# Performance work log

Hardware: AMD Instinct MI355X
Metric: run time of the kernel (lower is better)

## Reference

```python
import jax, jax.numpy as jnp
import numpy as np

B, S, D_IN, D_OUT, NUM_LAYERS = 128, 64, 2048, 2048, 64

def setup_inputs() -> dict:
    key = jax.random.key(0)
    k1, k2, k3 = jax.random.split(key, 3)
    x = jax.random.normal(k1, (B, S, D_IN), dtype=jnp.float32)
    weight = jax.random.normal(k2, (NUM_LAYERS, D_OUT, D_IN), dtype=jnp.float32)
    layer_idx = jax.random.randint(k3, (S,), 0, NUM_LAYERS, dtype=jnp.int32)
    return {"x": x, "weight": weight, "layer_idx": layer_idx}

def reference(x, weight, layer_idx):
    # x: [B, S, D_in]; weight: [L, D_out, D_in]; layer_idx: [S] ints in [0, L)
    # Per position s: out[:, s, :] = x[:, s, :] @ weight[layer_idx[s]].T
    w_sel = weight[layer_idx]                      # [S, D_out, D_in] gather
    out = jnp.einsum('bsd,sod->bso', x, w_sel)     # batched per-position GEMMs
    return out
```

## Files before the change

### kernel.cpp

```cpp
#include <hip/hip_runtime.h>
#include <hip/hip_bf16.h>

#define B_DIM 128
#define S_DIM 64
#define DIN   2048
#define DOUT  2048
#define NLAYERS 64

#define BM 128
#define BN 128
#define BK 64
#define NK (DIN / BK)
#define NTILES (S_DIM * (DOUT / BN))
#define NXCD 8

typedef __bf16 bf16_t;
typedef __attribute__((ext_vector_type(8))) bf16_t bf16x8;
typedef __attribute__((ext_vector_type(4))) float f32x4;

__global__ void rank_sort(const int* __restrict__ layer_idx, int* __restrict__ perm) {
    __shared__ int L[S_DIM];
    const int s = threadIdx.x;
    L[s] = layer_idx[s];
    __syncthreads();
    const int mine = L[s];
    int rank = 0;
    #pragma unroll
    for (int t = 0; t < S_DIM; ++t) {
        const int lt = L[t];
        rank += (lt < mine || (lt == mine && t < s)) ? 1 : 0;
    }
    perm[rank] = s;
}

__launch_bounds__(256, 2)
__global__ void flex_linear_gemm(const float* __restrict__ x,
                                 const float* __restrict__ w,
                                 const int* __restrict__ layer_idx,
                                 const int* __restrict__ perm,
                                 float* __restrict__ out) {
    __shared__ bf16_t Alds[BM * BK];
    __shared__ bf16_t Blds[BN * BK];

    const int orig = blockIdx.x;
    const int xcd  = orig & (NXCD - 1);
    const int slot = orig >> 3;
    const int tile = xcd * (NTILES / NXCD) + slot;
    const int yy   = tile >> 4;
    const int nb   = tile & 15;

    const int s  = perm[yy];
    const int layer = layer_idx[s];

    const float* Ag = x + (size_t)s * DIN;
    const float* Bg = w + (size_t)layer * (size_t)(DOUT * DIN) + (size_t)(nb * BN) * DIN;

    const int tid  = threadIdx.x;
    const int lane = tid & 63;
    const int wave = tid >> 6;
    const int wr = (wave >> 1) * 64;
    const int wc = (wave & 1) * 64;
    const int lrow = lane & 15;
    const int lk   = (lane >> 4) * 8;

    int offW[4];
    const float* pA[4];
    const float* pB[4];
    #pragma unroll
    for (int i = 0; i < 4; ++i) {
        const int row = (tid >> 3) + 32 * i;
        const int kc8 = (tid & 7) * 8;
        offW[i] = (row * BK + kc8) ^ ((row & 7) << 3);
        pA[i] = Ag + (size_t)row * (S_DIM * DIN) + kc8;
        pB[i] = Bg + (size_t)row * DIN + kc8;
    }
    int offA[2][4], offB[2][4];
    #pragma unroll
    for (int kk = 0; kk < 2; ++kk) {
        #pragma unroll
        for (int m = 0; m < 4; ++m) {
            const int ra = wr + m * 16 + lrow;
            const int rb = wc + m * 16 + lrow;
            offA[kk][m] = (ra * BK + kk * 32 + lk) ^ ((ra & 7) << 3);
            offB[kk][m] = (rb * BK + kk * 32 + lk) ^ ((rb & 7) << 3);
        }
    }

    f32x4 RA[8], RB[8];
    f32x4 acc[4][4] = {};

    auto issue = [&](int kb) {
        const int koff = kb * BK;
        #pragma unroll
        for (int i = 0; i < 4; ++i) {
            const float* a = pA[i] + koff;
            const float* b = pB[i] + koff;
            RA[2 * i]     = *(const f32x4*)a;
            RA[2 * i + 1] = *(const f32x4*)(a + 4);
            RB[2 * i]     = *(const f32x4*)b;
            RB[2 * i + 1] = *(const f32x4*)(b + 4);
        }
    };
    auto cvt_write = [&]() {
        #pragma unroll
        for (int i = 0; i < 4; ++i) {
            bf16x8 va, vb;
            #pragma unroll
            for (int j = 0; j < 4; ++j) {
                va[j]     = (bf16_t)RA[2 * i][j];
                va[j + 4] = (bf16_t)RA[2 * i + 1][j];
                vb[j]     = (bf16_t)RB[2 * i][j];
                vb[j + 4] = (bf16_t)RB[2 * i + 1][j];
            }
            *(bf16x8*)&Alds[offW[i]] = va;
            *(bf16x8*)&Blds[offW[i]] = vb;
        }
    };
    auto compute = [&]() {
        #pragma unroll
        for (int kk = 0; kk < 2; ++kk) {
            bf16x8 af[4], bfr[4];
            #pragma unroll
            for (int m = 0; m < 4; ++m) {
                af[m]  = *(const bf16x8*)&Alds[offA[kk][m]];
                bfr[m] = *(const bf16x8*)&Blds[offB[kk][m]];
            }
            #pragma unroll
            for (int m = 0; m < 4; ++m)
                #pragma unroll
                for (int n = 0; n < 4; ++n)
                    acc[m][n] = __builtin_amdgcn_mfma_f32_16x16x32_bf16(af[m], bfr[n], acc[m][n], 0, 0, 0);
        }
    };

    issue(0);
    cvt_write();
    for (int kb = 0; kb < NK - 1; ++kb) {
        __syncthreads();
        issue(kb + 1);
        compute();
        __syncthreads();
        cvt_write();
    }
    __syncthreads();
    compute();

    float* Og = out + (size_t)s * DOUT + (size_t)(nb * BN);
    #pragma unroll
    for (int m = 0; m < 4; ++m) {
        const int rb = wr + m * 16 + (lane >> 4) * 4;
        #pragma unroll
        for (int r = 0; r < 4; ++r) {
            float* orow = Og + (size_t)(rb + r) * (S_DIM * DOUT);
            #pragma unroll
            for (int n = 0; n < 4; ++n)
                orow[wc + n * 16 + (lane & 15)] = acc[m][n][r];
        }
    }
}

extern "C" void kernel_launch(void* const* d_in, const int* in_sizes, int n_in,
                              void* d_out, int out_size, void* d_ws, size_t ws_size,
                              hipStream_t stream) {
    const float* x         = (const float*)d_in[0];
    const float* w         = (const float*)d_in[1];
    const int*   layer_idx = (const int*)d_in[2];
    float*       out       = (float*)d_out;
    int*         perm      = (int*)d_ws;

    rank_sort<<<1, S_DIM, 0, stream>>>(layer_idx, perm);
    flex_linear_gemm<<<NTILES, dim3(256), 0, stream>>>(x, w, layer_idx, perm, out);
}
```

Before: 277.0 us.

## Pre-convert x to bf16 in a separate pass and use nontemporal weight loads

Adds a pre-pass kernel that converts x from fp32 to bf16 into workspace, so the GEMM reads half the bytes for A and skips the per-tile conversion. Every x row is re-read by 16 N-tiles, so the conversion is done once instead of repeatedly. Weight loads and output stores now use nontemporal hints to reduce cache pollution. The cost is an extra kernel launch and one full pass over x (64 MB read, 32 MB write), and the fast path only runs if the workspace is large enough.

```diff
diff --git a/kernel.cpp b/kernel.cpp
--- a/kernel.cpp
+++ b/kernel.cpp
@@ -33,8 +33,23 @@
     perm[rank] = s;
 }
 
+__global__ void convert_x(const float* __restrict__ x, bf16_t* __restrict__ x16) {
+    const size_t i = ((size_t)blockIdx.x * 256 + threadIdx.x) * 8;
+    f32x4 a = *(const f32x4*)(x + i);
+    f32x4 b = *(const f32x4*)(x + i + 4);
+    bf16x8 v;
+    #pragma unroll
+    for (int j = 0; j < 4; ++j) { v[j] = (bf16_t)a[j]; v[j + 4] = (bf16_t)b[j]; }
+    *(bf16x8*)(x16 + i) = v;
+}
+
+template <typename T>
+__device__ __forceinline__ T ntload(const T* p) { return __builtin_nontemporal_load(p); }
+
+template <bool XBF16>
 __launch_bounds__(256, 2)
 __global__ void flex_linear_gemm(const float* __restrict__ x,
+                                 const bf16_t* __restrict__ x16,
                                  const float* __restrict__ w,
                                  const int* __restrict__ layer_idx,
                                  const int* __restrict__ perm,
@@ -52,7 +67,6 @@
     const int s  = perm[yy];
     const int layer = layer_idx[s];
 
-    const float* Ag = x + (size_t)s * DIN;
     const float* Bg = w + (size_t)layer * (size_t)(DOUT * DIN) + (size_t)(nb * BN) * DIN;
 
     const int tid  = threadIdx.x;
@@ -64,15 +78,18 @@
     const int lk   = (lane >> 4) * 8;
 
     int offW[4];
-    const float* pA[4];
-    const float* pB[4];
+    const float*  pA[4];
+    const bf16_t* pA16[4];
+    const float*  pB[4];
     #pragma unroll
     for (int i = 0; i < 4; ++i) {
         const int row = (tid >> 3) + 32 * i;
         const int kc8 = (tid & 7) * 8;
         offW[i] = (row * BK + kc8) ^ ((row & 7) << 3);
-        pA[i] = Ag + (size_t)row * (S_DIM * DIN) + kc8;
-        pB[i] = Bg + (size_t)row * DIN + kc8;
+        const size_t aoff = (size_t)row * (S_DIM * DIN) + (size_t)s * DIN + kc8;
+        pA[i]   = x   + aoff;
+        pA16[i] = x16 + aoff;
+        pB[i]   = Bg + (size_t)row * DIN + kc8;
     }
     int offA[2][4], offB[2][4];
     #pragma unroll
@@ -86,33 +103,47 @@
         }
     }
 
-    f32x4 RA[8], RB[8];
-    f32x4 acc[4][4] = {};
+    bf16x8 RA16[4];
+    f32x4  RA[8];
+    f32x4  RB[8];
+    f32x4  acc[4][4] = {};
 
     auto issue = [&](int kb) {
         const int koff = kb * BK;
         #pragma unroll
         for (int i = 0; i < 4; ++i) {
-            const float* a = pA[i] + koff;
+            if constexpr (XBF16) {
+                RA16[i] = *(const bf16x8*)(pA16[i] + koff);
+            } else {
+                const float* a = pA[i] + koff;
+                RA[2 * i]     = *(const f32x4*)a;
+                RA[2 * i + 1] = *(const f32x4*)(a + 4);
+            }
             const float* b = pB[i] + koff;
-            RA[2 * i]     = *(const f32x4*)a;
-            RA[2 * i + 1] = *(const f32x4*)(a + 4);
-            RB[2 * i]     = *(const f32x4*)b;
-            RB[2 * i + 1] = *(const f32x4*)(b + 4);
+            RB[2 * i]     = ntload((const f32x4*)b);
+            RB[2 * i + 1] = ntload((const f32x4*)(b + 4));
         }
     };
     auto cvt_write = [&]() {
         #pragma unroll
         for (int i = 0; i < 4; ++i) {
-            bf16x8 va, vb;
+            bf16x8 vb;
             #pragma unroll
             for (int j = 0; j < 4; ++j) {
-                va[j]     = (bf16_t)RA[2 * i][j];
-                va[j + 4] = (bf16_t)RA[2 * i + 1][j];
                 vb[j]     = (bf16_t)RB[2 * i][j];
                 vb[j + 4] = (bf16_t)RB[2 * i + 1][j];
             }
-            *(bf16x8*)&Alds[offW[i]] = va;
+            if constexpr (XBF16) {
+                *(bf16x8*)&Alds[offW[i]] = RA16[i];
+            } else {
+                bf16x8 va;
+                #pragma unroll
+                for (int j = 0; j < 4; ++j) {
+                    va[j]     = (bf16_t)RA[2 * i][j];
+                    va[j + 4] = (bf16_t)RA[2 * i + 1][j];
+                }
+                *(bf16x8*)&Alds[offW[i]] = va;
+            }
             *(bf16x8*)&Blds[offW[i]] = vb;
         }
     };
@@ -154,7 +185,7 @@
             float* orow = Og + (size_t)(rb + r) * (S_DIM * DOUT);
             #pragma unroll
             for (int n = 0; n < 4; ++n)
-                orow[wc + n * 16 + (lane & 15)] = acc[m][n][r];
+                __builtin_nontemporal_store(acc[m][n][r], &orow[wc + n * 16 + (lane & 15)]);
         }
     }
 }
@@ -166,8 +197,17 @@
     const float* w         = (const float*)d_in[1];
     const int*   layer_idx = (const int*)d_in[2];
     float*       out       = (float*)d_out;
-    int*         perm      = (int*)d_ws;
+
+    int*    perm = (int*)d_ws;
+    bf16_t* x16  = (bf16_t*)((char*)d_ws + 512);
+    const size_t need = 512 + (size_t)B_DIM * S_DIM * DIN * sizeof(bf16_t);
 
     rank_sort<<<1, S_DIM, 0, stream>>>(layer_idx, perm);
-    flex_linear_gemm<<<NTILES, dim3(256), 0, stream>>>(x, w, layer_idx, perm, out);
-}
+
+    if (ws_size >= need) {
+        convert_x<<<(B_DIM * S_DIM * DIN / 8) / 256, 256, 0, stream>>>(x, x16);
+        flex_linear_gemm<true><<<NTILES, dim3(256), 0, stream>>>(x, x16, w, layer_idx, perm, out);
+    } else {
+        flex_linear_gemm<false><<<NTILES, dim3(256), 0, stream>>>(x, x16, w, layer_idx, perm, out);
+    }
+}
```

New measurement: 279.6 us. No clear change (+0.9%).
